# Kernel tuning notes

Hardware: AMD Instinct MI355X
Metric: run time of the kernel (lower is better)

## Reference

```python
import jax, jax.numpy as jnp
import numpy as np

B, C_IN, C_KEY, C_VAL, C_OUT = 1, 64, 32, 64, 64
H = W = D = 64
SCALE = 8


def setup_inputs() -> dict:
    key = jax.random.key(0)
    ks = jax.random.split(key, 4)
    init = lambda k, shape, fan: jax.random.normal(k, shape, jnp.float32) * (fan ** -0.5)
    return {
        "x": jax.random.normal(ks[0], (B, C_IN, H, W, D), jnp.float32),
        "w_key": init(ks[1], (C_KEY, C_IN), C_IN),
        "b_key": jnp.zeros((C_KEY,), jnp.float32),
        "w_value": init(ks[2], (C_VAL, C_IN), C_IN),
        "b_value": jnp.zeros((C_VAL,), jnp.float32),
        "w_out": init(ks[3], (C_OUT, C_VAL), C_VAL),
        "b_out": jnp.zeros((C_OUT,), jnp.float32),
        "scale": SCALE,
    }


def _proj(t, wgt, bias):
    # 1x1x1 Conv3d == pointwise channel matmul
    return jnp.einsum('bchwd,oc->bohwd', t, wgt) + bias[None, :, None, None, None]


def _windows(t, s):
    # [B,C,H,W,D] -> [B, s^3 windows, hb*wb*db tokens, C]
    b, c, h, w, d = t.shape
    hb, wb, db = h // s, w // s, d // s
    t = t.reshape(b, c, s, hb, s, wb, s, db)
    t = t.transpose(0, 2, 4, 6, 3, 5, 7, 1)
    return t.reshape(b, s * s * s, hb * wb * db, c), (hb, wb, db)


def _unwindows(t, s, blk):
    hb, wb, db = blk
    b, c = t.shape[0], t.shape[-1]
    t = t.reshape(b, s, s, s, hb, wb, db, c)
    t = t.transpose(0, 7, 1, 4, 2, 5, 3, 6)
    return t.reshape(b, c, s * hb, s * wb, s * db)


def reference(x, w_key, b_key, w_value, b_value, w_out, b_out, scale):
    # f_query = f_key (shared module in the original)
    k_full = _proj(x, w_key, b_key)
    v_full = _proj(x, w_value, b_value)
    qw, blk = _windows(k_full, scale)
    kw = qw  # shared projection -> query == key
    vw, _ = _windows(v_full, scale)
    sim = jnp.einsum('bnlc,bnmc->bnlm', qw, kw) * (qw.shape[-1] ** -0.5)
    sim = jax.nn.softmax(sim, axis=-1)
    ctx = jnp.einsum('bnlm,bnmc->bnlc', sim, vw)
    ctx = _unwindows(ctx, scale, blk)
    return _proj(ctx, w_out, b_out)
```

## Files before the change

### kernel.cpp

```cpp
#include <hip/hip_runtime.h>

typedef unsigned short u16;
typedef __bf16 bf16x8 __attribute__((ext_vector_type(8)));
typedef float f32x4 __attribute__((ext_vector_type(4)));

union B8 {
    bf16x8 v;
    u16 s[8];
    unsigned u[4];
    uint4 u4;
};

__device__ __forceinline__ unsigned cvtpk(float a, float b) {
    unsigned r;
    asm("v_cvt_pk_bf16_f32 %0, %1, %2" : "=v"(r) : "v"(a), "v"(b));
    return r;
}
__device__ __forceinline__ float ex2(float x) {
    return __builtin_amdgcn_exp2f(x);
}
__device__ __forceinline__ B8 load_w8(const float* __restrict__ p, float s) {
    float4 lo = ((const float4*)p)[0];
    float4 hi = ((const float4*)p)[1];
    B8 r;
    r.u[0] = cvtpk(lo.x * s, lo.y * s);
    r.u[1] = cvtpk(lo.z * s, lo.w * s);
    r.u[2] = cvtpk(hi.x * s, hi.y * s);
    r.u[3] = cvtpk(hi.z * s, hi.w * s);
    return r;
}
__device__ __forceinline__ f32x4 mfma16(const B8 a, const B8 b, f32x4 c) {
    return __builtin_amdgcn_mfma_f32_16x16x32_bf16(a.v, b.v, c, 0, 0, 0);
}
__device__ __forceinline__ int kidx(int tok, int slot) {
    return tok * 32 + ((slot ^ ((tok >> 1) & 3)) << 3);
}

#define KOFF 0
#define VOFF 16384
#define POFF 49664
#define NSM  70144

__global__ __launch_bounds__(512, 1)
void psab_fused(const float* __restrict__ x,
                const float* __restrict__ wk, const float* __restrict__ bk,
                const float* __restrict__ wv, const float* __restrict__ bv,
                const float* __restrict__ wo, const float* __restrict__ bo,
                float* __restrict__ out)
{
    __shared__ __align__(16) u16 smem[NSM];
    const int t    = threadIdx.x;
    const int lane = t & 63;
    const int wid  = t >> 6;
    const int lr   = lane & 15;
    const int lq   = lane >> 4;

    const int bid = blockIdx.x;
    const int n   = (bid & 7) * 64 + (bid >> 3);
    const int sh = n >> 6, sw = (n >> 3) & 7, sd = n & 7;
    const size_t base_vox = (size_t)(sh * 8) * 4096 + (size_t)(sw * 8) * 64 + (size_t)(sd * 8);

    const float WSC = 0.50506330f;

    B8 wkB[2][2], wvB[2][4];
#pragma unroll
    for (int kt = 0; kt < 2; ++kt)
#pragma unroll
        for (int nt = 0; nt < 2; ++nt)
            wkB[kt][nt] = load_w8(wk + (nt * 16 + lr) * 64 + kt * 32 + lq * 8, WSC);
#pragma unroll
    for (int kt = 0; kt < 2; ++kt)
#pragma unroll
        for (int nt = 0; nt < 4; ++nt)
            wvB[kt][nt] = load_w8(wv + (nt * 16 + lr) * 64 + kt * 32 + lq * 8, 1.0f);
    float kbias[2], vbias[4];
#pragma unroll
    for (int nt = 0; nt < 2; ++nt) kbias[nt] = bk[nt * 16 + lr] * WSC;
#pragma unroll
    for (int nt = 0; nt < 4; ++nt) vbias[nt] = bv[nt * 16 + lr];

    const f32x4 z = {0.f, 0.f, 0.f, 0.f};

    const int cS = t & 63;
    const int r2 = t >> 6;
    float4 Lo[2], Hi[2];
#define LDX(cc)                                                                   \
    _Pragma("unroll")                                                             \
    for (int half = 0; half < 2; ++half) {                                        \
        const int rr = r2 + half * 8;                                             \
        const int hb = (cc) * 2 + (rr >> 3);                                      \
        const int wb = rr & 7;                                                    \
        const float* gp = x + (size_t)cS * 262144 + base_vox + hb * 4096 + wb * 64; \
        Lo[half] = ((const float4*)gp)[0];                                        \
        Hi[half] = ((const float4*)gp)[1];                                        \
    }

    LDX(0)
    for (int cc = 0; cc < 4; ++cc) {
        __syncthreads();
#pragma unroll
        for (int half = 0; half < 2; ++half) {
            const int rr = r2 + half * 8;
            unsigned a0 = cvtpk(Lo[half].x, Lo[half].y);
            unsigned a1 = cvtpk(Lo[half].z, Lo[half].w);
            unsigned a2 = cvtpk(Hi[half].x, Hi[half].y);
            unsigned a3 = cvtpk(Hi[half].z, Hi[half].w);
            u16* xp = &smem[POFF + (rr * 8) * 72 + cS];
            xp[0 * 72] = (u16)a0; xp[1 * 72] = (u16)(a0 >> 16);
            xp[2 * 72] = (u16)a1; xp[3 * 72] = (u16)(a1 >> 16);
            xp[4 * 72] = (u16)a2; xp[5 * 72] = (u16)(a2 >> 16);
            xp[6 * 72] = (u16)a3; xp[7 * 72] = (u16)(a3 >> 16);
        }
        __syncthreads();
        if (cc < 3) { LDX(cc + 1) }
        B8 xa[2];
        const int tokA = wid * 16 + lr;
        xa[0].u4 = *(const uint4*)&smem[POFF + tokA * 72 + 0 * 32 + lq * 8];
        xa[1].u4 = *(const uint4*)&smem[POFF + tokA * 72 + 1 * 32 + lq * 8];
        const int tg = cc * 128 + wid * 16 + lq * 4;
#pragma unroll
        for (int nt = 0; nt < 2; ++nt) {
            f32x4 kd = z;
            kd = mfma16(xa[0], wkB[0][nt], kd);
            kd = mfma16(xa[1], wkB[1][nt], kd);
            const int slot = nt * 2 + (lr >> 3);
            const int cko  = lr & 7;
            unsigned p01 = cvtpk(kd[0] + kbias[nt], kd[1] + kbias[nt]);
            unsigned p23 = cvtpk(kd[2] + kbias[nt], kd[3] + kbias[nt]);
            smem[KOFF + kidx(tg + 0, slot) + cko] = (u16)p01;
            smem[KOFF + kidx(tg + 1, slot) + cko] = (u16)(p01 >> 16);
            smem[KOFF + kidx(tg + 2, slot) + cko] = (u16)p23;
            smem[KOFF + kidx(tg + 3, slot) + cko] = (u16)(p23 >> 16);
        }
#pragma unroll
        for (int nt = 0; nt < 4; ++nt) {
            f32x4 vd = z;
            vd = mfma16(xa[0], wvB[0][nt], vd);
            vd = mfma16(xa[1], wvB[1][nt], vd);
            const int cv = nt * 16 + lr;
            uint2 pk;
            pk.x = cvtpk(vd[0] + vbias[nt], vd[1] + vbias[nt]);
            pk.y = cvtpk(vd[2] + vbias[nt], vd[3] + vbias[nt]);
            *(uint2*)&smem[VOFF + cv * 520 + tg] = pk;
        }
    }
    __syncthreads();

    B8 qb[4];
#pragma unroll
    for (int nt = 0; nt < 4; ++nt)
        qb[nt].u4 = *(const uint4*)&smem[KOFF + kidx(wid * 64 + nt * 16 + lr, lq)];

    B8 ones;
    ones.u[0] = 0x3f803f80u; ones.u[1] = 0x3f803f80u;
    ones.u[2] = 0x3f803f80u; ones.u[3] = 0x3f803f80u;

    f32x4 ctx[4][4], lacc[4];
#pragma unroll
    for (int nt = 0; nt < 4; ++nt) {
        lacc[nt] = z;
#pragma unroll
        for (int ct = 0; ct < 4; ++ct) ctx[ct][nt] = z;
    }
    const int prow = POFF + wid * 2560;

#pragma unroll 2
    for (int ci = 0; ci < 16; ++ci) {
        const int m0 = ci * 32;
        B8 ka0, ka1;
        ka0.u4 = *(const uint4*)&smem[KOFF + kidx(m0 + lr, lq)];
        ka1.u4 = *(const uint4*)&smem[KOFF + kidx(m0 + 16 + lr, lq)];
#pragma unroll
        for (int nt = 0; nt < 4; ++nt) {
            f32x4 s0 = mfma16(ka0, qb[nt], z);
            f32x4 s1 = mfma16(ka1, qb[nt], z);
            uint2 pkA, pkB;
            pkA.x = cvtpk(ex2(s0[0]), ex2(s0[1]));
            pkA.y = cvtpk(ex2(s0[2]), ex2(s0[3]));
            pkB.x = cvtpk(ex2(s1[0]), ex2(s1[1]));
            pkB.y = cvtpk(ex2(s1[2]), ex2(s1[3]));
            u16* pr = &smem[prow + (nt * 16 + lr) * 40];
            *(uint2*)&pr[0 * 16 + lq * 4] = pkA;
            *(uint2*)&pr[1 * 16 + lq * 4] = pkB;
        }
        B8 va[4], pb[4];
#pragma unroll
        for (int ct = 0; ct < 4; ++ct)
            va[ct].u4 = *(const uint4*)&smem[VOFF + (ct * 16 + lr) * 520 + m0 + lq * 8];
#pragma unroll
        for (int nt = 0; nt < 4; ++nt)
            pb[nt].u4 = *(const uint4*)&smem[prow + (nt * 16 + lr) * 40 + lq * 8];
#pragma unroll
        for (int nt = 0; nt < 4; ++nt)
            lacc[nt] = mfma16(ones, pb[nt], lacc[nt]);
#pragma unroll
        for (int ct = 0; ct < 4; ++ct)
#pragma unroll
            for (int nt = 0; nt < 4; ++nt)
                ctx[ct][nt] = mfma16(va[ct], pb[nt], ctx[ct][nt]);
    }

    __syncthreads();

    const int SLOT = wid * 8192;
#pragma unroll
    for (int nt = 0; nt < 4; ++nt) {
        const float inv = 1.0f / lacc[nt][0];
        u16* cr = &smem[SLOT + (nt * 16 + lr) * 72];
#pragma unroll
        for (int ct = 0; ct < 4; ++ct) {
            f32x4 c4 = ctx[ct][nt];
            uint2 pk;
            pk.x = cvtpk(c4[0] * inv, c4[1] * inv);
            pk.y = cvtpk(c4[2] * inv, c4[3] * inv);
            *(uint2*)&cr[ct * 16 + lq * 4] = pk;
        }
    }
    B8 woA[4][2], cbf[2][4];
#pragma unroll
    for (int mt = 0; mt < 4; ++mt)
#pragma unroll
        for (int kt = 0; kt < 2; ++kt)
            woA[mt][kt] = load_w8(wo + (mt * 16 + lr) * 64 + kt * 32 + lq * 8, 1.0f);
#pragma unroll
    for (int kt = 0; kt < 2; ++kt)
#pragma unroll
        for (int nt = 0; nt < 4; ++nt)
            cbf[kt][nt].u4 = *(const uint4*)&smem[SLOT + (nt * 16 + lr) * 72 + kt * 32 + lq * 8];

    float* fout = (float*)&smem[SLOT];
#pragma unroll
    for (int mt = 0; mt < 4; ++mt) {
        const float4 b4 = *(const float4*)(bo + mt * 16 + lq * 4);
#pragma unroll
        for (int nt = 0; nt < 4; ++nt) {
            f32x4 od = z;
            od = mfma16(woA[mt][0], cbf[0][nt], od);
            od = mfma16(woA[mt][1], cbf[1][nt], od);
            const int col = nt * 16 + lr;
            fout[(mt * 16 + lq * 4 + 0) * 64 + col] = od[0] + b4.x;
            fout[(mt * 16 + lq * 4 + 1) * 64 + col] = od[1] + b4.y;
            fout[(mt * 16 + lq * 4 + 2) * 64 + col] = od[2] + b4.z;
            fout[(mt * 16 + lq * 4 + 3) * 64 + col] = od[3] + b4.w;
        }
    }
    float* outw = out + base_vox + (size_t)wid * 4096;
#pragma unroll
    for (int it = 0; it < 16; ++it) {
        const int co = it * 4 + lq;
        const float4 v4 = *(const float4*)&fout[co * 64 + lr * 4];
        const int wb = lr >> 1, db0 = (lr & 1) * 4;
        *(float4*)&outw[(size_t)co * 262144 + wb * 64 + db0] = v4;
    }
}

extern "C" void kernel_launch(void* const* d_in, const int* in_sizes, int n_in,
                              void* d_out, int out_size, void* d_ws, size_t ws_size,
                              hipStream_t stream) {
    const float* x  = (const float*)d_in[0];
    const float* wk = (const float*)d_in[1];
    const float* bk = (const float*)d_in[2];
    const float* wv = (const float*)d_in[3];
    const float* bv = (const float*)d_in[4];
    const float* wo = (const float*)d_in[5];
    const float* bo = (const float*)d_in[6];
    float* o = (float*)d_out;
    psab_fused<<<dim3(512), dim3(512), 0, stream>>>(x, wk, bk, wv, bv, wo, bo, o);
}
```

Before: 76.98 us.

## Switch fused windowed attention to 32x32x16 MFMA with register-resident P

Replaces the 16x16x32 bf16 MFMA tiles with 32x32x16 tiles throughout the projection, attention and output stages. The probability tile is now repacked in registers using v_permlane32_swap instead of a round trip through LDS, and row sums come from scalar accumulation plus a cross-half shuffle instead of a ones-matrix MFMA. X staging loads larger chunks in two phases with fewer barriers, and the normalized context feeds the output projection straight from registers. The aim is to cut LDS traffic, barriers and MFMA instruction count, at the cost of higher register pressure from the 16-wide accumulators.

```diff
diff --git a/kernel.cpp b/kernel.cpp
--- a/kernel.cpp
+++ b/kernel.cpp
@@ -2,22 +2,18 @@
 
 typedef unsigned short u16;
 typedef __bf16 bf16x8 __attribute__((ext_vector_type(8)));
-typedef float f32x4 __attribute__((ext_vector_type(4)));
-
-union B8 {
-    bf16x8 v;
-    u16 s[8];
-    unsigned u[4];
-    uint4 u4;
-};
+typedef float f32x16 __attribute__((ext_vector_type(16)));
+
+union B8 { bf16x8 v; u16 s[8]; unsigned u[4]; uint4 u4; };
 
 __device__ __forceinline__ unsigned cvtpk(float a, float b) {
     unsigned r;
     asm("v_cvt_pk_bf16_f32 %0, %1, %2" : "=v"(r) : "v"(a), "v"(b));
     return r;
 }
-__device__ __forceinline__ float ex2(float x) {
-    return __builtin_amdgcn_exp2f(x);
+__device__ __forceinline__ float ex2(float x) { return __builtin_amdgcn_exp2f(x); }
+__device__ __forceinline__ void swap32(unsigned &a, unsigned &b) {
+    asm("v_permlane32_swap_b32 %0, %1" : "+v"(a), "+v"(b));
 }
 __device__ __forceinline__ B8 load_w8(const float* __restrict__ p, float s) {
     float4 lo = ((const float4*)p)[0];
@@ -29,17 +25,25 @@
     r.u[3] = cvtpk(hi.z * s, hi.w * s);
     return r;
 }
-__device__ __forceinline__ f32x4 mfma16(const B8 a, const B8 b, f32x4 c) {
-    return __builtin_amdgcn_mfma_f32_16x16x32_bf16(a.v, b.v, c, 0, 0, 0);
-}
-__device__ __forceinline__ int kidx(int tok, int slot) {
-    return tok * 32 + ((slot ^ ((tok >> 1) & 3)) << 3);
-}
-
-#define KOFF 0
+__device__ __forceinline__ f32x16 mfma32(const B8 a, const B8 b, f32x16 c) {
+    return __builtin_amdgcn_mfma_f32_32x32x16_bf16(a.v, b.v, c, 0, 0, 0);
+}
+__device__ __forceinline__ int kidx(int row, int sl) {
+    return row * 32 + (((sl ^ (row >> 1)) & 3) << 3);
+}
+__device__ __forceinline__ void build_b(const float* p, B8& b0, B8& b1) {
+    unsigned c0 = cvtpk(p[0], p[1]),   c1 = cvtpk(p[2], p[3]);
+    unsigned c2 = cvtpk(p[4], p[5]),   c3 = cvtpk(p[6], p[7]);
+    unsigned c4 = cvtpk(p[8], p[9]),   c5 = cvtpk(p[10], p[11]);
+    unsigned c6 = cvtpk(p[12], p[13]), c7 = cvtpk(p[14], p[15]);
+    swap32(c0, c2); swap32(c1, c3); swap32(c4, c6); swap32(c5, c7);
+    b0.u[0] = c0; b0.u[1] = c1; b0.u[2] = c2; b0.u[3] = c3;
+    b1.u[0] = c4; b1.u[1] = c5; b1.u[2] = c6; b1.u[3] = c7;
+}
+
 #define VOFF 16384
-#define POFF 49664
-#define NSM  70144
+#define XOFF 49664
+#define NSM  68096
 
 __global__ __launch_bounds__(512, 1)
 void psab_fused(const float* __restrict__ x,
@@ -52,8 +56,8 @@
     const int t    = threadIdx.x;
     const int lane = t & 63;
     const int wid  = t >> 6;
-    const int lr   = lane & 15;
-    const int lq   = lane >> 4;
+    const int cl   = lane & 31;
+    const int h5   = lane >> 5;
 
     const int bid = blockIdx.x;
     const int n   = (bid & 7) * 64 + (bid >> 3);
@@ -62,189 +66,187 @@
 
     const float WSC = 0.50506330f;
 
-    B8 wkB[2][2], wvB[2][4];
-#pragma unroll
-    for (int kt = 0; kt < 2; ++kt)
-#pragma unroll
-        for (int nt = 0; nt < 2; ++nt)
-            wkB[kt][nt] = load_w8(wk + (nt * 16 + lr) * 64 + kt * 32 + lq * 8, WSC);
-#pragma unroll
-    for (int kt = 0; kt < 2; ++kt)
-#pragma unroll
-        for (int nt = 0; nt < 4; ++nt)
-            wvB[kt][nt] = load_w8(wv + (nt * 16 + lr) * 64 + kt * 32 + lq * 8, 1.0f);
-    float kbias[2], vbias[4];
-#pragma unroll
-    for (int nt = 0; nt < 2; ++nt) kbias[nt] = bk[nt * 16 + lr] * WSC;
-#pragma unroll
-    for (int nt = 0; nt < 4; ++nt) vbias[nt] = bv[nt * 16 + lr];
-
-    const f32x4 z = {0.f, 0.f, 0.f, 0.f};
+    B8 wkB[4], wvB[2][4];
+#pragma unroll
+    for (int kc = 0; kc < 4; ++kc)
+        wkB[kc] = load_w8(wk + cl * 64 + kc * 16 + h5 * 8, WSC);
+#pragma unroll
+    for (int nb = 0; nb < 2; ++nb)
+#pragma unroll
+        for (int kc = 0; kc < 4; ++kc)
+            wvB[nb][kc] = load_w8(wv + (nb * 32 + cl) * 64 + kc * 16 + h5 * 8, 1.0f);
+    const float kbias = bk[cl] * WSC;
+    const float vbias[2] = { bv[cl], bv[32 + cl] };
+
+    const f32x16 z16 = {0,0,0,0,0,0,0,0,0,0,0,0,0,0,0,0};
 
     const int cS = t & 63;
     const int r2 = t >> 6;
-    float4 Lo[2], Hi[2];
-#define LDX(cc)                                                                   \
-    _Pragma("unroll")                                                             \
-    for (int half = 0; half < 2; ++half) {                                        \
-        const int rr = r2 + half * 8;                                             \
-        const int hb = (cc) * 2 + (rr >> 3);                                      \
-        const int wb = rr & 7;                                                    \
-        const float* gp = x + (size_t)cS * 262144 + base_vox + hb * 4096 + wb * 64; \
-        Lo[half] = ((const float4*)gp)[0];                                        \
-        Hi[half] = ((const float4*)gp)[1];                                        \
+    float4 L4[4], H4[4];
+#define LDX(cc)                                                                              \
+    _Pragma("unroll")                                                                        \
+    for (int i = 0; i < 4; ++i) {                                                            \
+        const float* gp = x + (size_t)cS * 262144 + base_vox + ((cc) * 4 + i) * 4096 + r2 * 64; \
+        L4[i] = ((const float4*)gp)[0];                                                      \
+        H4[i] = ((const float4*)gp)[1];                                                      \
+    }
+#define STX()                                                                                \
+    _Pragma("unroll")                                                                        \
+    for (int i = 0; i < 4; ++i) {                                                            \
+        unsigned a0 = cvtpk(L4[i].x, L4[i].y), a1 = cvtpk(L4[i].z, L4[i].w);                 \
+        unsigned a2 = cvtpk(H4[i].x, H4[i].y), a3 = cvtpk(H4[i].z, H4[i].w);                 \
+        u16* xp = &smem[XOFF + (i * 64 + r2 * 8) * 72 + cS];                                 \
+        xp[0 * 72] = (u16)a0; xp[1 * 72] = (u16)(a0 >> 16);                                  \
+        xp[2 * 72] = (u16)a1; xp[3 * 72] = (u16)(a1 >> 16);                                  \
+        xp[4 * 72] = (u16)a2; xp[5 * 72] = (u16)(a2 >> 16);                                  \
+        xp[6 * 72] = (u16)a3; xp[7 * 72] = (u16)(a3 >> 16);                                  \
     }
 
     LDX(0)
-    for (int cc = 0; cc < 4; ++cc) {
-        __syncthreads();
-#pragma unroll
-        for (int half = 0; half < 2; ++half) {
-            const int rr = r2 + half * 8;
-            unsigned a0 = cvtpk(Lo[half].x, Lo[half].y);
-            unsigned a1 = cvtpk(Lo[half].z, Lo[half].w);
-            unsigned a2 = cvtpk(Hi[half].x, Hi[half].y);
-            unsigned a3 = cvtpk(Hi[half].z, Hi[half].w);
-            u16* xp = &smem[POFF + (rr * 8) * 72 + cS];
-            xp[0 * 72] = (u16)a0; xp[1 * 72] = (u16)(a0 >> 16);
-            xp[2 * 72] = (u16)a1; xp[3 * 72] = (u16)(a1 >> 16);
-            xp[4 * 72] = (u16)a2; xp[5 * 72] = (u16)(a2 >> 16);
-            xp[6 * 72] = (u16)a3; xp[7 * 72] = (u16)(a3 >> 16);
-        }
-        __syncthreads();
-        if (cc < 3) { LDX(cc + 1) }
-        B8 xa[2];
-        const int tokA = wid * 16 + lr;
-        xa[0].u4 = *(const uint4*)&smem[POFF + tokA * 72 + 0 * 32 + lq * 8];
-        xa[1].u4 = *(const uint4*)&smem[POFF + tokA * 72 + 1 * 32 + lq * 8];
-        const int tg = cc * 128 + wid * 16 + lq * 4;
-#pragma unroll
-        for (int nt = 0; nt < 2; ++nt) {
-            f32x4 kd = z;
-            kd = mfma16(xa[0], wkB[0][nt], kd);
-            kd = mfma16(xa[1], wkB[1][nt], kd);
-            const int slot = nt * 2 + (lr >> 3);
-            const int cko  = lr & 7;
-            unsigned p01 = cvtpk(kd[0] + kbias[nt], kd[1] + kbias[nt]);
-            unsigned p23 = cvtpk(kd[2] + kbias[nt], kd[3] + kbias[nt]);
-            smem[KOFF + kidx(tg + 0, slot) + cko] = (u16)p01;
-            smem[KOFF + kidx(tg + 1, slot) + cko] = (u16)(p01 >> 16);
-            smem[KOFF + kidx(tg + 2, slot) + cko] = (u16)p23;
-            smem[KOFF + kidx(tg + 3, slot) + cko] = (u16)(p23 >> 16);
-        }
-#pragma unroll
-        for (int nt = 0; nt < 4; ++nt) {
-            f32x4 vd = z;
-            vd = mfma16(xa[0], wvB[0][nt], vd);
-            vd = mfma16(xa[1], wvB[1][nt], vd);
-            const int cv = nt * 16 + lr;
-            uint2 pk;
-            pk.x = cvtpk(vd[0] + vbias[nt], vd[1] + vbias[nt]);
-            pk.y = cvtpk(vd[2] + vbias[nt], vd[3] + vbias[nt]);
-            *(uint2*)&smem[VOFF + cv * 520 + tg] = pk;
-        }
-    }
+    STX()
     __syncthreads();
-
-    B8 qb[4];
-#pragma unroll
-    for (int nt = 0; nt < 4; ++nt)
-        qb[nt].u4 = *(const uint4*)&smem[KOFF + kidx(wid * 64 + nt * 16 + lr, lq)];
-
-    B8 ones;
-    ones.u[0] = 0x3f803f80u; ones.u[1] = 0x3f803f80u;
-    ones.u[2] = 0x3f803f80u; ones.u[3] = 0x3f803f80u;
-
-    f32x4 ctx[4][4], lacc[4];
-#pragma unroll
-    for (int nt = 0; nt < 4; ++nt) {
-        lacc[nt] = z;
-#pragma unroll
-        for (int ct = 0; ct < 4; ++ct) ctx[ct][nt] = z;
-    }
-    const int prow = POFF + wid * 2560;
+    LDX(1)
+
+#pragma unroll
+    for (int cc = 0; cc < 2; ++cc) {
+        const int tokb = cc * 256 + wid * 32;
+        B8 ax[4];
+#pragma unroll
+        for (int kc = 0; kc < 4; ++kc)
+            ax[kc].u4 = *(const uint4*)&smem[XOFF + (wid * 32 + cl) * 72 + kc * 16 + h5 * 8];
+        f32x16 kd = mfma32(ax[0], wkB[0], z16);
+        kd = mfma32(ax[1], wkB[1], kd);
+        kd = mfma32(ax[2], wkB[2], kd);
+        kd = mfma32(ax[3], wkB[3], kd);
+#pragma unroll
+        for (int r = 0; r < 16; ++r) {
+            const int row = tokb + (r & 3) + 8 * (r >> 2) + 4 * h5;
+            smem[kidx(row, cl >> 3) + (cl & 7)] = (u16)cvtpk(kd[r] + kbias, kd[r] + kbias);
+        }
+#pragma unroll
+        for (int nb = 0; nb < 2; ++nb) {
+            f32x16 vd = mfma32(ax[0], wvB[nb][0], z16);
+            vd = mfma32(ax[1], wvB[nb][1], vd);
+            vd = mfma32(ax[2], wvB[nb][2], vd);
+            vd = mfma32(ax[3], wvB[nb][3], vd);
+            const int cv = nb * 32 + cl;
+            const float vb = vbias[nb];
+#pragma unroll
+            for (int rq = 0; rq < 4; ++rq) {
+                uint2 pk;
+                pk.x = cvtpk(vd[rq * 4 + 0] + vb, vd[rq * 4 + 1] + vb);
+                pk.y = cvtpk(vd[rq * 4 + 2] + vb, vd[rq * 4 + 3] + vb);
+                *(uint2*)&smem[VOFF + cv * 520 + tokb + rq * 8 + 4 * h5] = pk;
+            }
+        }
+        if (cc == 0) {
+            __syncthreads();
+            STX()
+            __syncthreads();
+        }
+    }
+    __syncthreads();
+
+    B8 qB[2][2];
+#pragma unroll
+    for (int qb = 0; qb < 2; ++qb)
+#pragma unroll
+        for (int kc = 0; kc < 2; ++kc)
+            qB[qb][kc].u4 = *(const uint4*)&smem[kidx(wid * 64 + qb * 32 + cl, 2 * kc + h5)];
+
+    f32x16 ctx00 = z16, ctx01 = z16, ctx10 = z16, ctx11 = z16;
+    float lsum0 = 0.f, lsum1 = 0.f;
 
 #pragma unroll 2
     for (int ci = 0; ci < 16; ++ci) {
         const int m0 = ci * 32;
-        B8 ka0, ka1;
-        ka0.u4 = *(const uint4*)&smem[KOFF + kidx(m0 + lr, lq)];
-        ka1.u4 = *(const uint4*)&smem[KOFF + kidx(m0 + 16 + lr, lq)];
-#pragma unroll
-        for (int nt = 0; nt < 4; ++nt) {
-            f32x4 s0 = mfma16(ka0, qb[nt], z);
-            f32x4 s1 = mfma16(ka1, qb[nt], z);
-            uint2 pkA, pkB;
-            pkA.x = cvtpk(ex2(s0[0]), ex2(s0[1]));
-            pkA.y = cvtpk(ex2(s0[2]), ex2(s0[3]));
-            pkB.x = cvtpk(ex2(s1[0]), ex2(s1[1]));
-            pkB.y = cvtpk(ex2(s1[2]), ex2(s1[3]));
-            u16* pr = &smem[prow + (nt * 16 + lr) * 40];
-            *(uint2*)&pr[0 * 16 + lq * 4] = pkA;
-            *(uint2*)&pr[1 * 16 + lq * 4] = pkB;
-        }
-        B8 va[4], pb[4];
-#pragma unroll
-        for (int ct = 0; ct < 4; ++ct)
-            va[ct].u4 = *(const uint4*)&smem[VOFF + (ct * 16 + lr) * 520 + m0 + lq * 8];
-#pragma unroll
-        for (int nt = 0; nt < 4; ++nt)
-            pb[nt].u4 = *(const uint4*)&smem[prow + (nt * 16 + lr) * 40 + lq * 8];
-#pragma unroll
-        for (int nt = 0; nt < 4; ++nt)
-            lacc[nt] = mfma16(ones, pb[nt], lacc[nt]);
-#pragma unroll
-        for (int ct = 0; ct < 4; ++ct)
-#pragma unroll
-            for (int nt = 0; nt < 4; ++nt)
-                ctx[ct][nt] = mfma16(va[ct], pb[nt], ctx[ct][nt]);
-    }
+        B8 kA0, kA1, va00, va01, va10, va11;
+        kA0.u4 = *(const uint4*)&smem[kidx(m0 + cl, h5)];
+        kA1.u4 = *(const uint4*)&smem[kidx(m0 + cl, 2 + h5)];
+        va00.u4 = *(const uint4*)&smem[VOFF + cl * 520 + m0 + h5 * 8];
+        va01.u4 = *(const uint4*)&smem[VOFF + cl * 520 + m0 + 16 + h5 * 8];
+        va10.u4 = *(const uint4*)&smem[VOFF + (32 + cl) * 520 + m0 + h5 * 8];
+        va11.u4 = *(const uint4*)&smem[VOFF + (32 + cl) * 520 + m0 + 16 + h5 * 8];
+
+        f32x16 s0 = mfma32(kA0, qB[0][0], z16);
+        s0 = mfma32(kA1, qB[0][1], s0);
+        f32x16 s1 = mfma32(kA0, qB[1][0], z16);
+        s1 = mfma32(kA1, qB[1][1], s1);
+
+        float p[16];
+        B8 pb00, pb01, pb10, pb11;
+#pragma unroll
+        for (int i = 0; i < 16; ++i) p[i] = ex2(s0[i]);
+        lsum0 += (((p[0]+p[1])+(p[2]+p[3]))+((p[4]+p[5])+(p[6]+p[7])))
+               + (((p[8]+p[9])+(p[10]+p[11]))+((p[12]+p[13])+(p[14]+p[15])));
+        build_b(p, pb00, pb01);
+#pragma unroll
+        for (int i = 0; i < 16; ++i) p[i] = ex2(s1[i]);
+        lsum1 += (((p[0]+p[1])+(p[2]+p[3]))+((p[4]+p[5])+(p[6]+p[7])))
+               + (((p[8]+p[9])+(p[10]+p[11]))+((p[12]+p[13])+(p[14]+p[15])));
+        build_b(p, pb10, pb11);
+
+        ctx00 = mfma32(va00, pb00, ctx00); ctx00 = mfma32(va01, pb01, ctx00);
+        ctx10 = mfma32(va10, pb00, ctx10); ctx10 = mfma32(va11, pb01, ctx10);
+        ctx01 = mfma32(va00, pb10, ctx01); ctx01 = mfma32(va01, pb11, ctx01);
+        ctx11 = mfma32(va10, pb10, ctx11); ctx11 = mfma32(va11, pb11, ctx11);
+    }
+
+    lsum0 += __shfl_xor(lsum0, 32);
+    lsum1 += __shfl_xor(lsum1, 32);
+    const float inv0 = 1.0f / lsum0;
+    const float inv1 = 1.0f / lsum1;
+
+    B8 aw[2][4];
+#pragma unroll
+    for (int cob = 0; cob < 2; ++cob)
+#pragma unroll
+        for (int kc = 0; kc < 4; ++kc)
+            aw[cob][kc] = load_w8(wo + (cob * 32 + cl) * 64 + kc * 16 + h5 * 8, 1.0f);
+
+    float pn[16];
+    B8 cq0[4], cq1[4];
+#pragma unroll
+    for (int i = 0; i < 16; ++i) pn[i] = ctx00[i] * inv0;
+    build_b(pn, cq0[0], cq0[1]);
+#pragma unroll
+    for (int i = 0; i < 16; ++i) pn[i] = ctx10[i] * inv0;
+    build_b(pn, cq0[2], cq0[3]);
+#pragma unroll
+    for (int i = 0; i < 16; ++i) pn[i] = ctx01[i] * inv1;
+    build_b(pn, cq1[0], cq1[1]);
+#pragma unroll
+    for (int i = 0; i < 16; ++i) pn[i] = ctx11[i] * inv1;
+    build_b(pn, cq1[2], cq1[3]);
 
     __syncthreads();
 
-    const int SLOT = wid * 8192;
-#pragma unroll
-    for (int nt = 0; nt < 4; ++nt) {
-        const float inv = 1.0f / lacc[nt][0];
-        u16* cr = &smem[SLOT + (nt * 16 + lr) * 72];
-#pragma unroll
-        for (int ct = 0; ct < 4; ++ct) {
-            f32x4 c4 = ctx[ct][nt];
-            uint2 pk;
-            pk.x = cvtpk(c4[0] * inv, c4[1] * inv);
-            pk.y = cvtpk(c4[2] * inv, c4[3] * inv);
-            *(uint2*)&cr[ct * 16 + lq * 4] = pk;
-        }
-    }
-    B8 woA[4][2], cbf[2][4];
-#pragma unroll
-    for (int mt = 0; mt < 4; ++mt)
-#pragma unroll
-        for (int kt = 0; kt < 2; ++kt)
-            woA[mt][kt] = load_w8(wo + (mt * 16 + lr) * 64 + kt * 32 + lq * 8, 1.0f);
-#pragma unroll
-    for (int kt = 0; kt < 2; ++kt)
-#pragma unroll
-        for (int nt = 0; nt < 4; ++nt)
-            cbf[kt][nt].u4 = *(const uint4*)&smem[SLOT + (nt * 16 + lr) * 72 + kt * 32 + lq * 8];
-
-    float* fout = (float*)&smem[SLOT];
-#pragma unroll
-    for (int mt = 0; mt < 4; ++mt) {
-        const float4 b4 = *(const float4*)(bo + mt * 16 + lq * 4);
-#pragma unroll
-        for (int nt = 0; nt < 4; ++nt) {
-            f32x4 od = z;
-            od = mfma16(woA[mt][0], cbf[0][nt], od);
-            od = mfma16(woA[mt][1], cbf[1][nt], od);
-            const int col = nt * 16 + lr;
-            fout[(mt * 16 + lq * 4 + 0) * 64 + col] = od[0] + b4.x;
-            fout[(mt * 16 + lq * 4 + 1) * 64 + col] = od[1] + b4.y;
-            fout[(mt * 16 + lq * 4 + 2) * 64 + col] = od[2] + b4.z;
-            fout[(mt * 16 + lq * 4 + 3) * 64 + col] = od[3] + b4.w;
-        }
-    }
+    float* fout = (float*)((char*)smem + wid * 16384);
+#pragma unroll
+    for (int cob = 0; cob < 2; ++cob) {
+        f32x16 od0 = mfma32(aw[cob][0], cq0[0], z16);
+        od0 = mfma32(aw[cob][1], cq0[1], od0);
+        od0 = mfma32(aw[cob][2], cq0[2], od0);
+        od0 = mfma32(aw[cob][3], cq0[3], od0);
+        f32x16 od1 = mfma32(aw[cob][0], cq1[0], z16);
+        od1 = mfma32(aw[cob][1], cq1[1], od1);
+        od1 = mfma32(aw[cob][2], cq1[2], od1);
+        od1 = mfma32(aw[cob][3], cq1[3], od1);
+#pragma unroll
+        for (int rq = 0; rq < 4; ++rq) {
+            const float4 b4 = *(const float4*)(bo + cob * 32 + rq * 8 + h5 * 4);
+            const float bb[4] = { b4.x, b4.y, b4.z, b4.w };
+#pragma unroll
+            for (int i = 0; i < 4; ++i) {
+                const int row = cob * 32 + rq * 8 + h5 * 4 + i;
+                fout[row * 64 + cl]      = od0[rq * 4 + i] + bb[i];
+                fout[row * 64 + 32 + cl] = od1[rq * 4 + i] + bb[i];
+            }
+        }
+    }
+
     float* outw = out + base_vox + (size_t)wid * 4096;
+    const int lq = lane >> 4, lr = lane & 15;
 #pragma unroll
     for (int it = 0; it < 16; ++it) {
         const int co = it * 4 + lq;
```

Measured after the change: 72.34 us. 6.0% less time.
